# Optimization experiments

Measured on AMD Instinct MI355X. Metric: run time of the kernel, lower is better.

## Reference

```python
import jax, jax.numpy as jnp
import numpy as np

INF = 1e10
EPS = 1e-5
B, N, F, H, NC, NRBF = 2, 512, 64, 64, 32, 50
GAMMA = 10.0  # RBF width for the continuous filter convolution kernel


def setup_inputs() -> dict:
    key = jax.random.key(0)
    ks = jax.random.split(key, 16)
    def lin(k, i, o):
        return (jax.random.normal(k, (i, o), jnp.float32) / np.sqrt(i)).astype(jnp.float32)
    d = {}
    d["h"] = jax.random.normal(ks[0], (B, N, F), jnp.float32)
    d["x"] = jax.random.normal(ks[1], (B, N, 3), jnp.float32)
    d["mask"] = jnp.ones((B, N, N), jnp.float32)
    # ContinuousFilterConvolution(2F -> H): feature branch + RBF filter branch
    d["W_dh"] = lin(ks[2], 2 * F, H); d["b_dh"] = jnp.zeros((H,), jnp.float32)
    d["mu"] = jnp.linspace(0.0, 5.0, NRBF).astype(jnp.float32)
    d["W_f"] = lin(ks[3], NRBF, H); d["b_f"] = jnp.zeros((H,), jnp.float32)
    # semantic_attention_mlp: Linear(2F,1,bias=False) + SiLU
    d["W_sa"] = lin(ks[4], 2 * F, 1)
    # edge_weight_mlp: Linear(2F+H, NC) + Tanh
    d["W_ew"] = lin(ks[5], 2 * F + H, NC); d["b_ew"] = jnp.zeros((NC,), jnp.float32)
    # post_norm_nlp: Linear(NC,H) SiLU Linear(H,H)
    d["W_pn1"] = lin(ks[6], NC, H); d["b_pn1"] = jnp.zeros((H,), jnp.float32)
    d["W_pn2"] = lin(ks[7], H, H); d["b_pn2"] = jnp.zeros((H,), jnp.float32)
    # node_mlp: Linear(2H+F,H) SiLU Linear(H,H)
    d["W_nm1"] = lin(ks[8], 2 * H + F, H); d["b_nm1"] = jnp.zeros((H,), jnp.float32)
    d["W_nm2"] = lin(ks[9], H, H); d["b_nm2"] = jnp.zeros((H,), jnp.float32)
    # coordinate_mlp: Linear(H,H) SiLU Linear(H,1)
    d["W_cm1"] = lin(ks[10], H, H); d["b_cm1"] = jnp.zeros((H,), jnp.float32)
    d["W_cm2"] = lin(ks[11], H, 1); d["b_cm2"] = jnp.zeros((1,), jnp.float32)
    return d


def reference(h, x, mask, W_dh, b_dh, mu, W_f, b_f, W_sa, W_ew, b_ew,
              W_pn1, b_pn1, W_pn2, b_pn2, W_nm1, b_nm1, W_nm2, b_nm2,
              W_cm1, b_cm1, W_cm2, b_cm2):
    silu = jax.nn.silu
    n = h.shape[-2]
    # pairwise displacements: entry [b,i,j] = x[b,j] - x[b,i]
    x_minus_xt = x[..., None, :, :] - x[..., :, None, :]                       # [B,N,N,3]
    norm = jnp.sqrt(jax.nn.relu(jnp.sum(x_minus_xt ** 2, -1, keepdims=True)) + EPS)  # [B,N,N,1]
    eye = jnp.eye(n, dtype=norm.dtype)[..., None]                              # [N,N,1]
    _norm = norm + INF * eye + (1.0 - mask[..., None]) * INF
    spatial = jax.nn.softmax(-_norm, axis=-2)                                  # softmin over senders
    # h_cat_ht[b,i,j] = concat(h[b,j], h[b,i])
    hi = jnp.broadcast_to(h[..., None, :, :], h.shape[:-2] + (n, n, h.shape[-1]))
    hj = jnp.broadcast_to(h[..., :, None, :], h.shape[:-2] + (n, n, h.shape[-1]))
    h_cat = jnp.concatenate([hi, hj], -1)                                      # [B,N,N,2F]
    # continuous filter convolution: feature MLP gated by RBF-expanded distance filter
    rbf = jnp.exp(-GAMMA * (norm - mu) ** 2)                                   # [B,N,N,NRBF]
    filtered = (h_cat @ W_dh + b_dh) * (rbf @ W_f + b_f)                       # [B,N,N,H]
    # semantic attention
    sem = silu(h_cat @ W_sa)                                                   # [B,N,N,1]
    sem = sem - INF * eye + (mask[..., None] - 1.0) * INF
    sem = jax.nn.softmax(sem, axis=-2)
    # per-edge coefficient weights on normalized displacement vectors
    w = jnp.tanh(jnp.concatenate([h_cat, filtered], -1) @ W_ew + b_ew)         # [B,N,N,NC]
    dirvec = x_minus_xt / (norm ** 2 + EPS)                                    # [B,N,N,3]
    att = w[..., None] * dirvec[..., None, :] * mask[..., None, None]          # [B,N,N,NC,3]
    att_sum = att.sum(-3)                                                      # sum over j -> [B,N,NC,3]
    att_norm = jnp.sqrt(jax.nn.relu(jnp.sum(att_sum ** 2, -1)) + EPS)          # [B,N,NC]
    emb = silu(att_norm @ W_pn1 + b_pn1) @ W_pn2 + b_pn2                       # [B,N,H]
    # edge messages and coordinate update
    h_e = filtered * mask[..., None]
    _h_e = (silu(h_e @ W_cm1 + b_cm1) @ W_cm2 + b_cm2) * mask[..., None]       # [B,N,N,1]
    _x = (x_minus_xt * _h_e).sum(-2) + x                                       # [B,N,3]
    # combined spatial*semantic attention and aggregation
    total = jax.nn.softmax(sem * spatial + (mask[..., None] - 1.0) * INF, axis=-2)
    h_e_agg = (total * h_e).sum(-2)                                            # [B,N,H]
    z = jnp.concatenate([h, h_e_agg, emb], -1)                                 # [B,N,F+2H]
    _h = silu(z @ W_nm1 + b_nm1) @ W_nm2 + b_nm2                               # [B,N,H]
    return _h, _x
```

## Files before the change

kernel.cpp:

```cpp
#include <hip/hip_runtime.h>

#define INF 1e10f
#define EPSV 1e-5f
#define NB 2
#define NN 512
#define NF 64
#define NH 64
#define NCC 32
#define NRBF 50
#define NND (NB*NN)
#define MU_STEP (5.0f/49.0f)
#define C20S (20.f*MU_STEP)

typedef _Float16 half8 __attribute__((ext_vector_type(8)));
typedef float f32x4 __attribute__((ext_vector_type(4)));

__device__ __forceinline__ float frcp(float x){ return __builtin_amdgcn_rcpf(x); }
__device__ __forceinline__ float silu_f(float x){ return x * frcp(1.f + __expf(-x)); }
__device__ __forceinline__ float tanh_f(float x){
  float t = __expf(2.f * x);
  return fmaf(-2.f, frcp(t + 1.f), 1.f);
}

__device__ __forceinline__ float wredSum(float v){
  v += __shfl_down(v, 32); v += __shfl_down(v, 16); v += __shfl_down(v, 8);
  v += __shfl_down(v, 4);  v += __shfl_down(v, 2);  v += __shfl_down(v, 1);
  return v;
}
__device__ __forceinline__ float bredSum(float v, float* red, int tid){
  float w = wredSum(v);
  __syncthreads();
  if ((tid & 63) == 0) red[tid >> 6] = w;
  __syncthreads();
  return (red[0] + red[1]) + (red[2] + red[3]);
}
__device__ __forceinline__ float2 bredSum2(float a, float b, float* red, int tid){
  float wa = wredSum(a), wb = wredSum(b);
  __syncthreads();
  if ((tid & 63) == 0){ red[(tid >> 6) * 2] = wa; red[(tid >> 6) * 2 + 1] = wb; }
  __syncthreads();
  return make_float2(red[0] + red[2] + red[4] + red[6],
                     red[1] + red[3] + red[5] + red[7]);
}

__global__ void kA(const float* __restrict__ h, const float* __restrict__ Wdh,
                   const float* __restrict__ Wew, const float* __restrict__ Wsa,
                   const float* __restrict__ bdh, const float* __restrict__ bew,
                   const float* __restrict__ Wf, const float* __restrict__ bf,
                   const float* __restrict__ Wcm1,
                   float* __restrict__ u, float* __restrict__ vb,
                   float* __restrict__ e1r, float* __restrict__ e2c,
                   float* __restrict__ s1, float* __restrict__ s2,
                   unsigned int* __restrict__ frag){
  const int tid = threadIdx.x;
  const int sub = tid >> 6, l = tid & 63;
  const int node = blockIdx.x * 4 + sub;
  __shared__ float sh[4][NF];
  sh[sub][l] = h[node * NF + l];
  __syncthreads();
  float ua = 0.f, va = 0.f;
  #pragma unroll
  for (int f = 0; f < NF; ++f){
    float hv = sh[sub][f];
    ua = fmaf(hv, Wdh[f * NH + l], ua);
    va = fmaf(hv, Wdh[(NF + f) * NH + l], va);
  }
  u[node * NH + l] = ua;
  vb[node * NH + l] = va + bdh[l];
  const int nc = l & 31;
  const int half = l >> 5;
  float ea = 0.f;
  #pragma unroll
  for (int f = 0; f < NF; ++f) ea = fmaf(sh[sub][f], Wew[(half * NF + f) * NCC + nc], ea);
  if (half == 0) e1r[node * NCC + nc] = ea;
  else           e2c[node * NCC + nc] = ea + bew[nc];
  if (l < 2){
    const float* wp = Wsa + l * NF;
    float s = 0.f;
    #pragma unroll
    for (int f = 0; f < NF; ++f) s = fmaf(sh[sub][f], wp[f], s);
    if (l == 0) s1[node] = s; else s2[node] = s;
  }
  if (blockIdx.x < 20){
    const int fi = blockIdx.x;
    const int lane = tid >> 2, dw = tid & 3;
    float v[2];
    #pragma unroll
    for (int e2 = 0; e2 < 2; ++e2){
      int e = dw * 2 + e2;
      int kk = 8 * (lane >> 4) + e;
      int n16 = lane & 15;
      float val;
      if (fi < 8){
        int mt = fi >> 1, kc = fi & 1;
        int hh = 8 * (n16 >> 2) + (n16 & 3) + 4 * (mt & 1) + 32 * (mt >> 1);
        int r = kk + 32 * kc;
        val = (r < NRBF) ? Wf[r * NH + hh] : ((r == NRBF) ? bf[hh] : 0.f);
      } else if (fi < 16){
        int q = fi - 8; int kc = q >> 2, nt = q & 3;
        val = Wcm1[(kk + 32 * kc) * NH + (n16 + 16 * nt)];
      } else {
        int q = fi - 16; int kc = q >> 1, n2 = q & 1;
        val = Wew[(2 * NF + kk + 32 * kc) * NCC + (n16 + 16 * n2)];
      }
      v[e2] = val;
    }
    unsigned int lo = (unsigned int)__builtin_bit_cast(unsigned short, (_Float16)v[0]);
    unsigned int hi = (unsigned int)__builtin_bit_cast(unsigned short, (_Float16)v[1]);
    frag[fi * 256 + lane * 4 + dw] = lo | (hi << 16);
  }
}

__global__ __launch_bounds__(256, 2) void kB(
    const float* __restrict__ x, const float* __restrict__ mask,
    const float* __restrict__ h_g,
    const float* __restrict__ u, const float* __restrict__ vb,
    const float* __restrict__ s1g, const float* __restrict__ s2g,
    const float* __restrict__ e1r, const float* __restrict__ e2c,
    const float* __restrict__ Wc2, const float* __restrict__ bc1, const float* __restrict__ bc2g,
    const unsigned int* __restrict__ frag,
    const float* __restrict__ Wpn1, const float* __restrict__ bpn1,
    const float* __restrict__ Wpn2, const float* __restrict__ bpn2,
    const float* __restrict__ Wnm1, const float* __restrict__ bnm1,
    const float* __restrict__ Wnm2, const float* __restrict__ bnm2,
    float* __restrict__ out)
{
  const int bid = blockIdx.x;
  const int b = bid >> 9, i = bid & (NN - 1);
  const int tid = threadIdx.x;
  const int lane = tid & 63, wave = tid >> 6;
  const int l15 = lane & 15, g = lane >> 4;
  const int base = b * NN;

  __shared__ __align__(16) float4 s_geo[NN];
  __shared__ __align__(16) float4 s_c[NN];
  __shared__ float s_m[NN];
  __shared__ float s_red[8];
  __shared__ half8 s_WB[20][64];

  {
    const int4* src = (const int4*)frag;
    int4* dst = (int4*)&s_WB[0][0];
    #pragma unroll
    for (int q = 0; q < 5; ++q) dst[tid + q * 256] = src[tid + q * 256];
  }

  const float xi0 = x[(base + i) * 3 + 0];
  const float xi1 = x[(base + i) * 3 + 1];
  const float xi2 = x[(base + i) * 3 + 2];
  const float s2i = s2g[base + i];

  float ea[2], es[2], mj[2];
  #pragma unroll
  for (int q = 0; q < 2; ++q){
    const int j = tid + q * 256;
    float d0 = x[(base + j) * 3 + 0] - xi0;
    float d1 = x[(base + j) * 3 + 1] - xi1;
    float d2 = x[(base + j) * 3 + 2] - xi2;
    float nsq = d0 * d0 + d1 * d1 + d2 * d2;
    float norm = sqrtf(fmaxf(nsq, 0.f) + EPSV);
    float m = mask[(base + i) * NN + j];
    float eye = (j == i) ? 1.f : 0.f;
    ea[q] = __expf(-(norm + eye * INF + (1.f - m) * INF));
    float sp = s1g[base + j] + s2i;
    es[q] = __expf(silu_f(sp) - eye * INF + (m - 1.f) * INF);
    s_geo[j] = make_float4(d0 * m, d1 * m, d2 * m, norm);
    s_m[j] = m;
    float inv = frcp(norm * norm + EPSV) * m;
    s_c[j] = make_float4(d0 * inv, d1 * inv, d2 * inv, 0.f);
    mj[q] = m;
  }
  float2 S12 = bredSum2(ea[0] + ea[1], es[0] + es[1], s_red, tid);
  const float iS1 = 1.f / S12.x, iS2 = 1.f / S12.y;
  float e3[2];
  #pragma unroll
  for (int q = 0; q < 2; ++q)
    e3[q] = __expf((es[q] * iS2) * (ea[q] * iS1) + (mj[q] - 1.f) * INF);
  float S3 = bredSum(e3[0] + e3[1], s_red, tid);
  const float iS3 = 1.f / S3;
  s_c[tid].w       = e3[0] * iS3 * mj[0];
  s_c[tid + 256].w = e3[1] * iS3 * mj[1];
  __syncthreads();

  float vba[16];
  {
    const float4* vp = (const float4*)(vb + (size_t)(base + i) * NH);
    float4 a0 = vp[2*g], a1 = vp[2*g+1], a2 = vp[2*g+8], a3 = vp[2*g+9];
    vba[0]=a0.x; vba[1]=a0.y; vba[2]=a0.z; vba[3]=a0.w;
    vba[4]=a1.x; vba[5]=a1.y; vba[6]=a1.z; vba[7]=a1.w;
    vba[8]=a2.x; vba[9]=a2.y; vba[10]=a2.z; vba[11]=a2.w;
    vba[12]=a3.x; vba[13]=a3.y; vba[14]=a3.z; vba[15]=a3.w;
  }
  float wc2v[4], bc1v[4];
  #pragma unroll
  for (int nt = 0; nt < 4; ++nt){ wc2v[nt] = Wc2[l15 + 16*nt]; bc1v[nt] = bc1[l15 + 16*nt]; }
  float e2v[2];
  e2v[0] = e2c[(size_t)(base + i) * NCC + l15];
  e2v[1] = e2c[(size_t)(base + i) * NCC + l15 + 16];
  const float bc2v16 = bc2g[0] * 0.0625f;
  const float mub0 = (float)(8 * g) * MU_STEP;
  const float mub1 = (float)(8 * g + 32) * MU_STEP;
  const float QCONST = __expf(-20.f * MU_STEP * MU_STEP);
  const float crho0 = -10.f * MU_STEP * MU_STEP * (float)(16 * g + 1);
  const float crho1 = -10.f * MU_STEP * MU_STEP * (float)(16 * g + 65);

  float hg[16];
  #pragma unroll
  for (int e = 0; e < 16; ++e) hg[e] = 0.f;
  float at[2][3] = {{0.f,0.f,0.f},{0.f,0.f,0.f}};
  float xa0 = 0.f, xa1 = 0.f, xa2 = 0.f;

  float4 u0, u1, u2, u3;
  {
    const float4* up = (const float4*)(u + (size_t)(base + wave*128 + l15) * NH);
    u0 = up[2*g]; u1 = up[2*g+1]; u2 = up[2*g+8]; u3 = up[2*g+9];
  }

  for (int jt8 = 0; jt8 < 8; ++jt8){
    const int jt = wave * 128 + jt8 * 16;
    const int jl = jt + l15;
    float normj = s_geo[jl].w;
    float tmw = s_c[jl].w;
    half8 brb[2];
    {
      float d0 = normj - mub0;
      float d1 = normj - mub1;
      float e0 = __expf(-10.f * d0 * d0);
      float e1 = __expf(-10.f * d1 * d1);
      float r0a = __expf(fmaf(C20S, normj, crho0));
      float r1a = __expf(fmaf(C20S, normj, crho1));
      const int rbase1 = 8*g + 32;
      brb[0][0] = (_Float16)e0;
      brb[1][0] = (_Float16)((rbase1 < NRBF) ? e1 : ((rbase1 == NRBF) ? 1.f : 0.f));
      #pragma unroll
      for (int rr = 1; rr < 8; ++rr){
        e0 *= r0a;  r0a *= QCONST;
        e1 *= r1a;  r1a *= QCONST;
        int r1i = rbase1 + rr;
        brb[0][rr] = (_Float16)e0;
        brb[1][rr] = (_Float16)((r1i < NRBF) ? e1 : ((r1i == NRBF) ? 1.f : 0.f));
      }
    }
    f32x4 fc[4];
    __builtin_amdgcn_s_setprio(1);
    #pragma unroll
    for (int mt = 0; mt < 4; ++mt){
      f32x4 z = {0.f,0.f,0.f,0.f};
      z = __builtin_amdgcn_mfma_f32_16x16x32_f16(s_WB[2*mt][lane],   brb[0], z, 0, 0, 0);
      z = __builtin_amdgcn_mfma_f32_16x16x32_f16(s_WB[2*mt+1][lane], brb[1], z, 0, 0, 0);
      fc[mt] = z;
    }
    __builtin_amdgcn_s_setprio(0);
    float ua[16] = {u0.x,u0.y,u0.z,u0.w, u1.x,u1.y,u1.z,u1.w,
                    u2.x,u2.y,u2.z,u2.w, u3.x,u3.y,u3.z,u3.w};
    float FH[16];
    half8 afh[2];
    #pragma unroll
    for (int kc = 0; kc < 2; ++kc)
      #pragma unroll
      for (int e = 0; e < 8; ++e){
        int el = kc*8 + e;
        float f = fc[2*kc + (e>>2)][e & 3];
        FH[el] = (ua[el] + vba[el]) * f;
        afh[kc][e] = (_Float16)FH[el];
      }
    {
      const int jn = (jt8 < 7) ? (jl + 16) : jl;
      const float4* upn = (const float4*)(u + (size_t)(base + jn) * NH);
      u0 = upn[2*g]; u1 = upn[2*g+1]; u2 = upn[2*g+8]; u3 = upn[2*g+9];
    }
    #pragma unroll
    for (int e = 0; e < 16; ++e) hg[e] = fmaf(tmw, FH[e], hg[e]);
    float e1v[4][2];
    #pragma unroll
    for (int reg = 0; reg < 4; ++reg){
      const float* ep1 = e1r + (size_t)(base + jt + 4*g + reg) * NCC + l15;
      e1v[reg][0] = ep1[0]; e1v[reg][1] = ep1[16];
    }
    f32x4 cm[4];
    f32x4 ew[2];
    __builtin_amdgcn_s_setprio(1);
    #pragma unroll
    for (int nt = 0; nt < 4; ++nt){
      f32x4 z = {0.f,0.f,0.f,0.f};
      z = __builtin_amdgcn_mfma_f32_16x16x32_f16(afh[0], s_WB[8+nt][lane],  z, 0, 0, 0);
      z = __builtin_amdgcn_mfma_f32_16x16x32_f16(afh[1], s_WB[12+nt][lane], z, 0, 0, 0);
      cm[nt] = z;
    }
    #pragma unroll
    for (int n2 = 0; n2 < 2; ++n2){
      f32x4 z = {0.f,0.f,0.f,0.f};
      z = __builtin_amdgcn_mfma_f32_16x16x32_f16(afh[0], s_WB[16+n2][lane], z, 0, 0, 0);
      z = __builtin_amdgcn_mfma_f32_16x16x32_f16(afh[1], s_WB[18+n2][lane], z, 0, 0, 0);
      ew[n2] = z;
    }
    __builtin_amdgcn_s_setprio(0);
    float mreg[4]; float4 geo4[4], c4[4];
    #pragma unroll
    for (int reg = 0; reg < 4; ++reg){
      int jr = jt + 4*g + reg;
      mreg[reg] = s_m[jr];
      geo4[reg] = s_geo[jr];
      c4[reg]   = s_c[jr];
    }
    float hEp[4] = {0.f,0.f,0.f,0.f};
    #pragma unroll
    for (int nt = 0; nt < 4; ++nt)
      #pragma unroll
      for (int reg = 0; reg < 4; ++reg){
        float tv = silu_f(fmaf(mreg[reg], cm[nt][reg], bc1v[nt]));
        hEp[reg] = fmaf(tv, wc2v[nt], hEp[reg]);
      }
    #pragma unroll
    for (int reg = 0; reg < 4; ++reg){
      float hv = hEp[reg] + bc2v16;
      xa0 = fmaf(geo4[reg].x, hv, xa0);
      xa1 = fmaf(geo4[reg].y, hv, xa1);
      xa2 = fmaf(geo4[reg].z, hv, xa2);
    }
    #pragma unroll
    for (int n2 = 0; n2 < 2; ++n2)
      #pragma unroll
      for (int reg = 0; reg < 4; ++reg){
        float wv = tanh_f(ew[n2][reg] + e1v[reg][n2] + e2v[n2]);
        at[n2][0] = fmaf(wv, c4[reg].x, at[n2][0]);
        at[n2][1] = fmaf(wv, c4[reg].y, at[n2][1]);
        at[n2][2] = fmaf(wv, c4[reg].z, at[n2][2]);
      }
  }

  #pragma unroll
  for (int e = 0; e < 16; ++e){
    float v = hg[e];
    v += __shfl_xor(v, 1); v += __shfl_xor(v, 2);
    v += __shfl_xor(v, 4); v += __shfl_xor(v, 8);
    hg[e] = v;
  }
  #pragma unroll
  for (int n2 = 0; n2 < 2; ++n2)
    #pragma unroll
    for (int d = 0; d < 3; ++d){
      float v = at[n2][d];
      v += __shfl_xor(v, 16); v += __shfl_xor(v, 32);
      at[n2][d] = v;
    }
  #pragma unroll
  for (int s = 1; s <= 32; s <<= 1){
    xa0 += __shfl_xor(xa0, s);
    xa1 += __shfl_xor(xa1, s);
    xa2 += __shfl_xor(xa2, s);
  }

  __syncthreads();
  float* ep = (float*)&s_WB[0][0];
  if (l15 == 0){
    #pragma unroll
    for (int e = 0; e < 16; ++e)
      ep[wave*64 + 8*g + (e & 7) + 32*(e >> 3)] = hg[e];
  }
  if (lane < 16){
    #pragma unroll
    for (int n2 = 0; n2 < 2; ++n2)
      #pragma unroll
      for (int d = 0; d < 3; ++d)
        ep[256 + wave*96 + (l15 + 16*n2)*3 + d] = at[n2][d];
  }
  if (lane == 0){
    ep[640 + wave*3 + 0] = xa0; ep[640 + wave*3 + 1] = xa1; ep[640 + wave*3 + 2] = xa2;
  }
  __syncthreads();
  if (tid < 64)
    ep[832 + tid] = ep[tid] + ep[64+tid] + ep[128+tid] + ep[192+tid];
  if (tid >= 64 && tid < 160){
    int t = tid - 64;
    ep[704 + t] = ep[256+t] + ep[352+t] + ep[448+t] + ep[544+t];
  }
  if (tid >= 192 && tid < 195){
    int d = tid - 192;
    out[NB*NN*NH + (base + i)*3 + d] =
        ep[640+d] + ep[643+d] + ep[646+d] + ep[649+d] + x[(base + i)*3 + d];
  }
  __syncthreads();
  if (tid < 32){
    float a0 = ep[704 + tid*3], a1 = ep[704 + tid*3 + 1], a2 = ep[704 + tid*3 + 2];
    ep[896 + tid] = sqrtf(fmaxf(a0*a0 + a1*a1 + a2*a2, 0.f) + EPSV);
  }
  __syncthreads();

  if (wave == 0){
    const int k = lane;
    const int node = base + i;
    ep[1056 + k] = h_g[node * NF + k];
    asm volatile("s_waitcnt lgkmcnt(0)" ::: "memory");
    __builtin_amdgcn_wave_barrier();
    float acc = bpn1[k];
    #pragma unroll
    for (int t = 0; t < NCC; ++t) acc = fmaf(ep[896 + t], Wpn1[t * NH + k], acc);
    ep[928 + k] = silu_f(acc);
    asm volatile("s_waitcnt lgkmcnt(0)" ::: "memory");
    __builtin_amdgcn_wave_barrier();
    acc = bpn2[k];
    #pragma unroll
    for (int t = 0; t < NH; ++t) acc = fmaf(ep[928 + t], Wpn2[t * NH + k], acc);
    ep[992 + k] = acc;
    asm volatile("s_waitcnt lgkmcnt(0)" ::: "memory");
    __builtin_amdgcn_wave_barrier();
    acc = bnm1[k];
    #pragma unroll
    for (int t = 0; t < NF; ++t) acc = fmaf(ep[1056 + t], Wnm1[t * NH + k], acc);
    #pragma unroll
    for (int t = 0; t < NH; ++t) acc = fmaf(ep[832 + t],  Wnm1[(NF + t) * NH + k], acc);
    #pragma unroll
    for (int t = 0; t < NH; ++t) acc = fmaf(ep[992 + t],  Wnm1[(NF + NH + t) * NH + k], acc);
    float srv = silu_f(acc);
    asm volatile("s_waitcnt lgkmcnt(0)" ::: "memory");
    __builtin_amdgcn_wave_barrier();
    ep[928 + k] = srv;
    asm volatile("s_waitcnt lgkmcnt(0)" ::: "memory");
    __builtin_amdgcn_wave_barrier();
    acc = bnm2[k];
    #pragma unroll
    for (int t = 0; t < NH; ++t) acc = fmaf(ep[928 + t], Wnm2[t * NH + k], acc);
    out[node * NH + k] = acc;
  }
}

extern "C" void kernel_launch(void* const* d_in, const int* in_sizes, int n_in,
                              void* d_out, int out_size, void* d_ws, size_t ws_size,
                              hipStream_t stream){
  const float* h    = (const float*)d_in[0];
  const float* x    = (const float*)d_in[1];
  const float* mask = (const float*)d_in[2];
  const float* Wdh  = (const float*)d_in[3];
  const float* bdh  = (const float*)d_in[4];
  const float* Wf   = (const float*)d_in[6];
  const float* bf   = (const float*)d_in[7];
  const float* Wsa  = (const float*)d_in[8];
  const float* Wew  = (const float*)d_in[9];
  const float* bew  = (const float*)d_in[10];
  const float* Wpn1 = (const float*)d_in[11];
  const float* bpn1 = (const float*)d_in[12];
  const float* Wpn2 = (const float*)d_in[13];
  const float* bpn2 = (const float*)d_in[14];
  const float* Wnm1 = (const float*)d_in[15];
  const float* bnm1 = (const float*)d_in[16];
  const float* Wnm2 = (const float*)d_in[17];
  const float* bnm2 = (const float*)d_in[18];
  const float* Wcm1 = (const float*)d_in[19];
  const float* bcm1 = (const float*)d_in[20];
  const float* Wcm2 = (const float*)d_in[21];
  const float* bcm2 = (const float*)d_in[22];
  float* out = (float*)d_out;
  float* ws  = (float*)d_ws;

  float* u    = ws;
  float* vbuf = u    + 65536;
  float* s1   = vbuf + 65536;
  float* s2   = s1   + 1024;
  float* e1r  = s2   + 1024;
  float* e2c  = e1r  + 32768;
  unsigned int* fragb = (unsigned int*)(e2c + 32768);

  hipLaunchKernelGGL(kA, dim3(NND / 4), dim3(256), 0, stream,
                     h, Wdh, Wew, Wsa, bdh, bew, Wf, bf, Wcm1,
                     u, vbuf, e1r, e2c, s1, s2, fragb);
  hipLaunchKernelGGL(kB, dim3(NND), dim3(256), 0, stream,
                     x, mask, h, u, vbuf, s1, s2, e1r, e2c,
                     Wcm2, bcm1, bcm2, fragb,
                     Wpn1, bpn1, Wpn2, bpn2, Wnm1, bnm1, Wnm2, bnm2, out);
}
```

Baseline: 53.20 us.

## Shrink LDS and register footprint to raise kB occupancy

Raises the launch-bounds occupancy target from 2 to 5 blocks per SM. To fit, it drops the s_c and s_m shared arrays by encoding the mask in the sign of the stored norm and recomputing the direction scale with a reciprocal in the loop. The per-thread vb registers move to shared memory, and the software-prefetched u loads are replaced with in-loop loads. This trades more recomputation and less latency hiding per wave for more resident waves, and the tighter register cap risks spills.

```diff
diff --git a/kernel.cpp b/kernel.cpp
--- a/kernel.cpp
+++ b/kernel.cpp
@@ -111,7 +111,7 @@
   }
 }
 
-__global__ __launch_bounds__(256, 2) void kB(
+__global__ __launch_bounds__(256, 5) void kB(
     const float* __restrict__ x, const float* __restrict__ mask,
     const float* __restrict__ h_g,
     const float* __restrict__ u, const float* __restrict__ vb,
@@ -133,8 +133,8 @@
   const int base = b * NN;
 
   __shared__ __align__(16) float4 s_geo[NN];
-  __shared__ __align__(16) float4 s_c[NN];
-  __shared__ float s_m[NN];
+  __shared__ float s_tot[NN];
+  __shared__ float s_vb[64];
   __shared__ float s_red[8];
   __shared__ half8 s_WB[20][64];
 
@@ -143,6 +143,7 @@
     int4* dst = (int4*)&s_WB[0][0];
     #pragma unroll
     for (int q = 0; q < 5; ++q) dst[tid + q * 256] = src[tid + q * 256];
+    if (tid < 64) s_vb[tid] = vb[(size_t)(base + i) * NH + tid];
   }
 
   const float xi0 = x[(base + i) * 3 + 0];
@@ -164,10 +165,7 @@
     ea[q] = __expf(-(norm + eye * INF + (1.f - m) * INF));
     float sp = s1g[base + j] + s2i;
     es[q] = __expf(silu_f(sp) - eye * INF + (m - 1.f) * INF);
-    s_geo[j] = make_float4(d0 * m, d1 * m, d2 * m, norm);
-    s_m[j] = m;
-    float inv = frcp(norm * norm + EPSV) * m;
-    s_c[j] = make_float4(d0 * inv, d1 * inv, d2 * inv, 0.f);
+    s_geo[j] = make_float4(d0 * m, d1 * m, d2 * m, (m > 0.5f) ? norm : -norm);
     mj[q] = m;
   }
   float2 S12 = bredSum2(ea[0] + ea[1], es[0] + es[1], s_red, tid);
@@ -178,19 +176,10 @@
     e3[q] = __expf((es[q] * iS2) * (ea[q] * iS1) + (mj[q] - 1.f) * INF);
   float S3 = bredSum(e3[0] + e3[1], s_red, tid);
   const float iS3 = 1.f / S3;
-  s_c[tid].w       = e3[0] * iS3 * mj[0];
-  s_c[tid + 256].w = e3[1] * iS3 * mj[1];
-  __syncthreads();
-
-  float vba[16];
-  {
-    const float4* vp = (const float4*)(vb + (size_t)(base + i) * NH);
-    float4 a0 = vp[2*g], a1 = vp[2*g+1], a2 = vp[2*g+8], a3 = vp[2*g+9];
-    vba[0]=a0.x; vba[1]=a0.y; vba[2]=a0.z; vba[3]=a0.w;
-    vba[4]=a1.x; vba[5]=a1.y; vba[6]=a1.z; vba[7]=a1.w;
-    vba[8]=a2.x; vba[9]=a2.y; vba[10]=a2.z; vba[11]=a2.w;
-    vba[12]=a3.x; vba[13]=a3.y; vba[14]=a3.z; vba[15]=a3.w;
-  }
+  s_tot[tid]       = e3[0] * iS3 * mj[0];
+  s_tot[tid + 256] = e3[1] * iS3 * mj[1];
+  __syncthreads();
+
   float wc2v[4], bc1v[4];
   #pragma unroll
   for (int nt = 0; nt < 4; ++nt){ wc2v[nt] = Wc2[l15 + 16*nt]; bc1v[nt] = bc1[l15 + 16*nt]; }
@@ -210,17 +199,14 @@
   float at[2][3] = {{0.f,0.f,0.f},{0.f,0.f,0.f}};
   float xa0 = 0.f, xa1 = 0.f, xa2 = 0.f;
 
-  float4 u0, u1, u2, u3;
-  {
-    const float4* up = (const float4*)(u + (size_t)(base + wave*128 + l15) * NH);
-    u0 = up[2*g]; u1 = up[2*g+1]; u2 = up[2*g+8]; u3 = up[2*g+9];
-  }
-
   for (int jt8 = 0; jt8 < 8; ++jt8){
     const int jt = wave * 128 + jt8 * 16;
     const int jl = jt + l15;
-    float normj = s_geo[jl].w;
-    float tmw = s_c[jl].w;
+    const float4* up = (const float4*)(u + (size_t)(base + jl) * NH);
+    float4 u0 = up[2*g], u1 = up[2*g+1], u2 = up[2*g+8], u3 = up[2*g+9];
+    float encw = s_geo[jl].w;
+    float normj = fabsf(encw);
+    float tmw = s_tot[jl];
     half8 brb[2];
     {
       float d0 = normj - mub0;
@@ -251,6 +237,12 @@
       fc[mt] = z;
     }
     __builtin_amdgcn_s_setprio(0);
+    int vbi = 8 * g;
+    asm volatile("" : "+v"(vbi));
+    const float4* vb4 = (const float4*)(s_vb + vbi);
+    float4 b0v = vb4[0], b1v = vb4[1], b2v = vb4[8], b3v = vb4[9];
+    float bv[16] = {b0v.x,b0v.y,b0v.z,b0v.w, b1v.x,b1v.y,b1v.z,b1v.w,
+                    b2v.x,b2v.y,b2v.z,b2v.w, b3v.x,b3v.y,b3v.z,b3v.w};
     float ua[16] = {u0.x,u0.y,u0.z,u0.w, u1.x,u1.y,u1.z,u1.w,
                     u2.x,u2.y,u2.z,u2.w, u3.x,u3.y,u3.z,u3.w};
     float FH[16];
@@ -261,14 +253,9 @@
       for (int e = 0; e < 8; ++e){
         int el = kc*8 + e;
         float f = fc[2*kc + (e>>2)][e & 3];
-        FH[el] = (ua[el] + vba[el]) * f;
+        FH[el] = (ua[el] + bv[el]) * f;
         afh[kc][e] = (_Float16)FH[el];
       }
-    {
-      const int jn = (jt8 < 7) ? (jl + 16) : jl;
-      const float4* upn = (const float4*)(u + (size_t)(base + jn) * NH);
-      u0 = upn[2*g]; u1 = upn[2*g+1]; u2 = upn[2*g+8]; u3 = upn[2*g+9];
-    }
     #pragma unroll
     for (int e = 0; e < 16; ++e) hg[e] = fmaf(tmw, FH[e], hg[e]);
     float e1v[4][2];
@@ -295,13 +282,14 @@
       ew[n2] = z;
     }
     __builtin_amdgcn_s_setprio(0);
-    float mreg[4]; float4 geo4[4], c4[4];
+    float mreg[4], invr[4]; float4 geo4[4];
     #pragma unroll
     for (int reg = 0; reg < 4; ++reg){
       int jr = jt + 4*g + reg;
-      mreg[reg] = s_m[jr];
       geo4[reg] = s_geo[jr];
-      c4[reg]   = s_c[jr];
+      float ew_ = geo4[reg].w;
+      mreg[reg] = (ew_ > 0.f) ? 1.f : 0.f;
+      invr[reg] = frcp(fmaf(ew_, ew_, EPSV));
     }
     float hEp[4] = {0.f,0.f,0.f,0.f};
     #pragma unroll
@@ -322,10 +310,10 @@
     for (int n2 = 0; n2 < 2; ++n2)
       #pragma unroll
       for (int reg = 0; reg < 4; ++reg){
-        float wv = tanh_f(ew[n2][reg] + e1v[reg][n2] + e2v[n2]);
-        at[n2][0] = fmaf(wv, c4[reg].x, at[n2][0]);
-        at[n2][1] = fmaf(wv, c4[reg].y, at[n2][1]);
-        at[n2][2] = fmaf(wv, c4[reg].z, at[n2][2]);
+        float wv = tanh_f(ew[n2][reg] + e1v[reg][n2] + e2v[n2]) * invr[reg];
+        at[n2][0] = fmaf(wv, geo4[reg].x, at[n2][0]);
+        at[n2][1] = fmaf(wv, geo4[reg].y, at[n2][1]);
+        at[n2][2] = fmaf(wv, geo4[reg].z, at[n2][2]);
       }
   }
 
```

Result: slower. 100.3 us (+88.5%).
